# Kernel tuning notes

Measured on AMD Instinct MI355X. Metric: run time of the kernel, lower is better.

The kernel has to match this reference:

```python
import jax, jax.numpy as jnp
import numpy as np

# QConv2D (AngleMap feature map, entanglement-free PQC model):
# each 3x3 patch value x_q is angle-encoded as RY(w_q * x_q) on qubit q,
# then n_layers of trainable RZ(a)/RY(b) rotations are applied; the layer
# outputs the Bloch vector (<X>,<Y>,<Z>) of every qubit -> 3*n_qubits values
# per patch. Channel outputs are summed (Add), filters concatenated, relu.

KERNEL = (3, 3)
STRIDE = (1, 1)


def _extract_patches(x, k, s):
    # x: (B,H,W,C) -> (B,i0,i1,C,K) with K = k0*k1
    B, H, W, C = x.shape
    i0 = (H - k[0]) // s[0] + 1
    i1 = (W - k[1]) // s[1] + 1
    ri = jnp.arange(i0)[:, None] * s[0] + jnp.arange(k[0])[None, :]  # (i0,k0)
    rj = jnp.arange(i1)[:, None] * s[1] + jnp.arange(k[1])[None, :]  # (i1,k1)
    p = x[:, ri]            # (B,i0,k0,W,C)
    p = p[:, :, :, rj]      # (B,i0,k0,i1,k1,C)
    p = jnp.transpose(p, (0, 1, 3, 5, 2, 4))  # (B,i0,i1,C,k0,k1)
    return p.reshape(B, i0, i1, C, k[0] * k[1])


def setup_inputs() -> dict:
    key = jax.random.key(0)
    k_x, k_w, k_a, k_b = jax.random.split(key, 4)
    B, H, W, C = 32, 128, 128, 3
    F, Q, L = 2, KERNEL[0] * KERNEL[1], 2  # filters, n_qubits, n_layers
    input_tensor = jax.random.uniform(k_x, (B, H, W, C), dtype=jnp.float32)
    w_enc = jax.random.normal(k_w, (F, C, Q), dtype=jnp.float32)
    a_rz = jax.random.normal(k_a, (F, C, L, Q), dtype=jnp.float32)
    b_ry = jax.random.normal(k_b, (F, C, L, Q), dtype=jnp.float32)
    return {"input_tensor": input_tensor, "w_enc": w_enc, "a_rz": a_rz, "b_ry": b_ry}


def reference(input_tensor, w_enc, a_rz, b_ry):
    B = input_tensor.shape[0]
    F, C, Q = w_enc.shape
    L = a_rz.shape[2]
    patches = _extract_patches(input_tensor, KERNEL, STRIDE)  # (B,i0,i1,C,Q)
    i0, i1 = patches.shape[1], patches.shape[2]
    # angle encoding per (filter, channel, qubit)
    theta = patches[:, :, :, None, :, :] * w_enc[None, None, None]  # (B,i0,i1,F,C,Q)
    vx, vy, vz = jnp.sin(theta), jnp.zeros_like(theta), jnp.cos(theta)
    for l in range(L):  # small fixed layer count
        ca, sa = jnp.cos(a_rz[:, :, l]), jnp.sin(a_rz[:, :, l])  # (F,C,Q)
        cb, sb = jnp.cos(b_ry[:, :, l]), jnp.sin(b_ry[:, :, l])
        # RZ(a): rotate Bloch vector about Z
        vx, vy = vx * ca - vy * sa, vx * sa + vy * ca
        # RY(b): rotate about Y
        vx, vz = vx * cb + vz * sb, -vx * sb + vz * cb
    out = jnp.stack([vx, vy, vz], axis=-1)       # (B,i0,i1,F,C,Q,3)
    out = out.sum(axis=4)                        # Add over channels -> (B,i0,i1,F,Q,3)
    out = out.reshape(B, i0, i1, F * Q * 3)      # Concatenate over filters
    return jax.nn.relu(out)
```

## Files before the change

kernel.cpp:

```cpp
#include <hip/hip_runtime.h>
#include <math.h>

#define NB 32
#define NH 128
#define NW 128
#define NC 3
#define NF 2
#define NQ 9
#define NL 2
#define I0 126
#define I1 126
#define NPIX (NB * I0 * I1)
#define NWORK (NPIX * 18)
#define GTHREADS 1016064
#define DPIX 56448
#define NITER 9

__global__ void precompute_tab(const float* __restrict__ w_enc,
                               const float* __restrict__ a_rz,
                               const float* __restrict__ b_ry,
                               float* __restrict__ tab) {
    int t = threadIdx.x;
    if (t >= NF * NC * NQ) return;
    int f = t / (NC * NQ);
    int c = (t / NQ) % NC;
    int q = t % NQ;

    float ux = 1.f, uy = 0.f, uz = 0.f;
    float wx = 0.f, wy = 0.f, wz = 1.f;
    for (int l = 0; l < NL; ++l) {
        int ia = ((f * NC + c) * NL + l) * NQ + q;
        float av = a_rz[ia], bv = b_ry[ia];
        float ca = cosf(av), sa = sinf(av);
        float cb = cosf(bv), sb = sinf(bv);
        float nx, ny, nz;
        nx = ux * ca - uy * sa; ny = ux * sa + uy * ca; ux = nx; uy = ny;
        nx = ux * cb + uz * sb; nz = -ux * sb + uz * cb; ux = nx; uz = nz;

        nx = wx * ca - wy * sa; ny = wx * sa + wy * ca; wx = nx; wy = ny;
        nx = wx * cb + wz * sb; nz = -wx * sb + wz * cb; wx = nx; wz = nz;
    }
    float* o = tab + t * 8;
    o[0] = w_enc[t];
    o[1] = ux; o[2] = uy; o[3] = uz;
    o[4] = wx; o[5] = wy; o[6] = wz;
    o[7] = 0.f;
}

struct f3 { float x, y, z; };

__global__ __launch_bounds__(256) void qconv_main(
        const float* __restrict__ x,
        const float* __restrict__ tab,
        float* __restrict__ out) {
    int T0 = blockIdx.x * 256 + threadIdx.x;
    int pixb = T0 / 18;
    int q18 = T0 - pixb * 18;
    int f = (q18 >= 9) ? 1 : 0;
    int q = q18 - f * 9;
    int di = q / 3, dj = q - di * 3;

    float cw[3], sx[3], sy[3], sz[3], cx[3], cy[3], cz[3];
#pragma unroll
    for (int c = 0; c < 3; ++c) {
        const float* r = tab + (size_t)(f * 27 + c * 9 + q) * 8;
        float4 v0 = *reinterpret_cast<const float4*>(r);
        float4 v1 = *reinterpret_cast<const float4*>(r + 4);
        cw[c] = v0.x; sx[c] = v0.y; sy[c] = v0.z; sz[c] = v0.w;
        cx[c] = v1.x; cy[c] = v1.y; cz[c] = v1.z;
    }

    int b   = pixb / (I0 * I1);
    int rem = pixb - b * (I0 * I1);
    int i   = rem / I1;
    int j   = rem - i * I1;

    int  icur   = i;
    long rowidx = (long)b * NH + i + di;
    long outidx = (long)pixb * 54 + q18 * 3;
    int  jcol   = j + dj;

    for (int it = 0; it < NITER; ++it) {
        const float* px = x + ((size_t)rowidx * NW + jcol) * NC;
        float p0 = px[0], p1 = px[1], p2 = px[2];

        float a0 = 0.f, a1 = 0.f, a2 = 0.f;
#pragma unroll
        for (int c = 0; c < 3; ++c) {
            float pc = (c == 0) ? p0 : (c == 1) ? p1 : p2;
            float s, co;
            __sincosf(pc * cw[c], &s, &co);
            a0 = fmaf(sx[c], s, fmaf(cx[c], co, a0));
            a1 = fmaf(sy[c], s, fmaf(cy[c], co, a1));
            a2 = fmaf(sz[c], s, fmaf(cz[c], co, a2));
        }

        f3 r;
        r.x = fmaxf(a0, 0.f);
        r.y = fmaxf(a1, 0.f);
        r.z = fmaxf(a2, 0.f);
        *reinterpret_cast<f3*>(out + outidx) = r;

        icur += 70;
        rowidx += 454;
        if (icur >= I0) { icur -= I0; rowidx += 2; }
        outidx += (long)DPIX * 54;
    }
}

extern "C" void kernel_launch(void* const* d_in, const int* in_sizes, int n_in,
                              void* d_out, int out_size, void* d_ws, size_t ws_size,
                              hipStream_t stream) {
    const float* x     = (const float*)d_in[0];
    const float* w_enc = (const float*)d_in[1];
    const float* a_rz  = (const float*)d_in[2];
    const float* b_ry  = (const float*)d_in[3];
    float* out = (float*)d_out;
    float* tab = (float*)d_ws;

    precompute_tab<<<1, 64, 0, stream>>>(w_enc, a_rz, b_ry, tab);

    int block = 256;
    int grid = GTHREADS / block;
    qconv_main<<<grid, block, 0, stream>>>(x, tab, out);
}
```

Baseline: 32.47 us.

## Fuse table precompute into main kernel and batch loads with native sin/cos

Drops the separate single-block precompute launch; each block now builds the rotation table in shared memory before the main loop. The encoding weights are pre-scaled by 1/(2π) so the hardware v_sin/v_cos builtins can be called directly, skipping the range reduction in __sincosf. The 9-iteration loop is unrolled in groups of three so three input loads are issued before any compute. The cost is redundant table work in every block, about 54 threads doing trig plus a __syncthreads, and possible loss of accuracy for large arguments.

```diff
diff --git a/kernel.cpp b/kernel.cpp
--- a/kernel.cpp
+++ b/kernel.cpp
@@ -14,46 +14,46 @@
 #define NWORK (NPIX * 18)
 #define GTHREADS 1016064
 #define DPIX 56448
-#define NITER 9
-
-__global__ void precompute_tab(const float* __restrict__ w_enc,
-                               const float* __restrict__ a_rz,
-                               const float* __restrict__ b_ry,
-                               float* __restrict__ tab) {
-    int t = threadIdx.x;
-    if (t >= NF * NC * NQ) return;
-    int f = t / (NC * NQ);
-    int c = (t / NQ) % NC;
-    int q = t % NQ;
-
-    float ux = 1.f, uy = 0.f, uz = 0.f;
-    float wx = 0.f, wy = 0.f, wz = 1.f;
-    for (int l = 0; l < NL; ++l) {
-        int ia = ((f * NC + c) * NL + l) * NQ + q;
-        float av = a_rz[ia], bv = b_ry[ia];
-        float ca = cosf(av), sa = sinf(av);
-        float cb = cosf(bv), sb = sinf(bv);
-        float nx, ny, nz;
-        nx = ux * ca - uy * sa; ny = ux * sa + uy * ca; ux = nx; uy = ny;
-        nx = ux * cb + uz * sb; nz = -ux * sb + uz * cb; ux = nx; uz = nz;
-
-        nx = wx * ca - wy * sa; ny = wx * sa + wy * ca; wx = nx; wy = ny;
-        nx = wx * cb + wz * sb; nz = -wx * sb + wz * cb; wx = nx; wz = nz;
-    }
-    float* o = tab + t * 8;
-    o[0] = w_enc[t];
-    o[1] = ux; o[2] = uy; o[3] = uz;
-    o[4] = wx; o[5] = wy; o[6] = wz;
-    o[7] = 0.f;
-}
+#define INV2PI 0.15915494309189535f
 
 struct f3 { float x, y, z; };
 
-__global__ __launch_bounds__(256) void qconv_main(
+__global__ __launch_bounds__(256) void qconv_fused(
         const float* __restrict__ x,
-        const float* __restrict__ tab,
+        const float* __restrict__ w_enc,
+        const float* __restrict__ a_rz,
+        const float* __restrict__ b_ry,
         float* __restrict__ out) {
-    int T0 = blockIdx.x * 256 + threadIdx.x;
+    __shared__ float stab[54 * 8];
+    int tid = threadIdx.x;
+    if (tid < 54) {
+        int t = tid;
+        int f = t / 27;
+        int c = (t / 9) % 3;
+        int q = t % 9;
+        float ux = 1.f, uy = 0.f, uz = 0.f;
+        float wx = 0.f, wy = 0.f, wz = 1.f;
+#pragma unroll
+        for (int l = 0; l < NL; ++l) {
+            int ia = ((f * NC + c) * NL + l) * NQ + q;
+            float sa, ca, sb, cb;
+            __sincosf(a_rz[ia], &sa, &ca);
+            __sincosf(b_ry[ia], &sb, &cb);
+            float nx, ny, nz;
+            nx = ux * ca - uy * sa; ny = ux * sa + uy * ca; ux = nx; uy = ny;
+            nx = ux * cb + uz * sb; nz = -ux * sb + uz * cb; ux = nx; uz = nz;
+            nx = wx * ca - wy * sa; ny = wx * sa + wy * ca; wx = nx; wy = ny;
+            nx = wx * cb + wz * sb; nz = -wx * sb + wz * cb; wx = nx; wz = nz;
+        }
+        float* o = stab + t * 8;
+        o[0] = w_enc[t] * INV2PI;
+        o[1] = ux; o[2] = uy; o[3] = uz;
+        o[4] = wx; o[5] = wy; o[6] = wz;
+        o[7] = 0.f;
+    }
+    __syncthreads();
+
+    int T0 = blockIdx.x * 256 + tid;
     int pixb = T0 / 18;
     int q18 = T0 - pixb * 18;
     int f = (q18 >= 9) ? 1 : 0;
@@ -63,7 +63,7 @@
     float cw[3], sx[3], sy[3], sz[3], cx[3], cy[3], cz[3];
 #pragma unroll
     for (int c = 0; c < 3; ++c) {
-        const float* r = tab + (size_t)(f * 27 + c * 9 + q) * 8;
+        const float* r = stab + (size_t)(f * 27 + c * 9 + q) * 8;
         float4 v0 = *reinterpret_cast<const float4*>(r);
         float4 v1 = *reinterpret_cast<const float4*>(r + 4);
         cw[c] = v0.x; sx[c] = v0.y; sy[c] = v0.z; sz[c] = v0.w;
@@ -75,37 +75,52 @@
     int i   = rem / I1;
     int j   = rem - i * I1;
 
-    int  icur   = i;
-    long rowidx = (long)b * NH + i + di;
-    long outidx = (long)pixb * 54 + q18 * 3;
-    int  jcol   = j + dj;
+    int icur = i;
+    const float* pin = x + ((size_t)((b * NH + i + di) * NW) + (j + dj)) * NC;
+    float* pout = out + (size_t)pixb * 54 + q18 * 3;
 
-    for (int it = 0; it < NITER; ++it) {
-        const float* px = x + ((size_t)rowidx * NW + jcol) * NC;
-        float p0 = px[0], p1 = px[1], p2 = px[2];
+    const long STEP_IN  = 454L * NW * NC;
+    const long WRAP_IN  = 2L * NW * NC;
+    const long STEP_OUT = (long)DPIX * 54;
 
-        float a0 = 0.f, a1 = 0.f, a2 = 0.f;
+#define ADVANCE()  do { icur += 70; pin += STEP_IN; \
+                        if (icur >= I0) { icur -= I0; pin += WRAP_IN; } } while (0)
+
+#define COMPUTE_STORE(P, OP) do {                                   \
+        float a0 = 0.f, a1 = 0.f, a2 = 0.f;                         \
+        _Pragma("unroll")                                           \
+        for (int c = 0; c < 3; ++c) {                               \
+            float pc = (c == 0) ? (P).x : (c == 1) ? (P).y : (P).z; \
+            float xr = pc * cw[c];                                  \
+            float s  = __builtin_amdgcn_sinf(xr);                   \
+            float co = __builtin_amdgcn_cosf(xr);                   \
+            a0 = fmaf(sx[c], s, fmaf(cx[c], co, a0));               \
+            a1 = fmaf(sy[c], s, fmaf(cy[c], co, a1));               \
+            a2 = fmaf(sz[c], s, fmaf(cz[c], co, a2));               \
+        }                                                           \
+        f3 r_;                                                      \
+        r_.x = fmaxf(a0, 0.f);                                      \
+        r_.y = fmaxf(a1, 0.f);                                      \
+        r_.z = fmaxf(a2, 0.f);                                      \
+        *reinterpret_cast<f3*>(OP) = r_;                            \
+    } while (0)
+
 #pragma unroll
-        for (int c = 0; c < 3; ++c) {
-            float pc = (c == 0) ? p0 : (c == 1) ? p1 : p2;
-            float s, co;
-            __sincosf(pc * cw[c], &s, &co);
-            a0 = fmaf(sx[c], s, fmaf(cx[c], co, a0));
-            a1 = fmaf(sy[c], s, fmaf(cy[c], co, a1));
-            a2 = fmaf(sz[c], s, fmaf(cz[c], co, a2));
-        }
+    for (int g = 0; g < 3; ++g) {
+        const float* pA = pin; ADVANCE();
+        const float* pB = pin; ADVANCE();
+        const float* pC = pin; ADVANCE();
+        f3 PA = *reinterpret_cast<const f3*>(pA);
+        f3 PB = *reinterpret_cast<const f3*>(pB);
+        f3 PC = *reinterpret_cast<const f3*>(pC);
 
-        f3 r;
-        r.x = fmaxf(a0, 0.f);
-        r.y = fmaxf(a1, 0.f);
-        r.z = fmaxf(a2, 0.f);
-        *reinterpret_cast<f3*>(out + outidx) = r;
-
-        icur += 70;
-        rowidx += 454;
-        if (icur >= I0) { icur -= I0; rowidx += 2; }
-        outidx += (long)DPIX * 54;
+        COMPUTE_STORE(PA, pout);
+        COMPUTE_STORE(PB, pout + STEP_OUT);
+        COMPUTE_STORE(PC, pout + 2 * STEP_OUT);
+        pout += 3 * STEP_OUT;
     }
+#undef ADVANCE
+#undef COMPUTE_STORE
 }
 
 extern "C" void kernel_launch(void* const* d_in, const int* in_sizes, int n_in,
@@ -116,11 +131,8 @@
     const float* a_rz  = (const float*)d_in[2];
     const float* b_ry  = (const float*)d_in[3];
     float* out = (float*)d_out;
-    float* tab = (float*)d_ws;
-
-    precompute_tab<<<1, 64, 0, stream>>>(w_enc, a_rz, b_ry, tab);
 
     int block = 256;
     int grid = GTHREADS / block;
-    qconv_main<<<grid, block, 0, stream>>>(x, tab, out);
+    qconv_fused<<<grid, block, 0, stream>>>(x, w_enc, a_rz, b_ry, out);
 }
```

Result: faster. 26.96 us (median of 2 runs) (-17.0%).
